# Optimization experiments

Measured on AMD Instinct MI355X. Metric: run time of the kernel, lower is better.

Reference implementation:

```python
import jax, jax.numpy as jnp
import numpy as np


def setup_inputs() -> dict:
    key = jax.random.key(0)
    x = jax.random.normal(key, (64, 512, 16, 16), dtype=jnp.float32)
    return {"x": x}


def reference(x):
    # x: [B, dim, h, w] -> covariance pooling y: [B, dim, dim]
    B, dim, h, w = x.shape
    M = h * w
    xf = x.reshape(B, dim, M)
    # I_hat = (1/M) I - (1/M^2) 11^T  (centering matrix scaled by 1/M)
    inv_M = jnp.asarray(1.0 / M, dtype=x.dtype)
    I_hat = inv_M * jnp.eye(M, dtype=x.dtype) - (inv_M * inv_M) * jnp.ones((M, M), dtype=x.dtype)
    # y = x @ I_hat @ x^T, I_hat broadcast over batch
    xI = jnp.einsum('bdm,mn->bdn', xf, I_hat)   # [B, dim, M]
    y = jnp.einsum('bdn,ben->bde', xI, xf)      # [B, dim, dim]
    return y
```

## Files before the change

### kernel.cpp

```cpp
#include <hip/hip_runtime.h>
#include <stdint.h>


typedef __attribute__((ext_vector_type(8))) short bf16x8;
typedef __attribute__((ext_vector_type(4))) float f32x4;

static __device__ __forceinline__ unsigned short f2bf(float f) {
    union { float f; uint32_t u; } c; c.f = f;
    uint32_t u = c.u;
    return (unsigned short)((u + 0x7FFFu + ((u >> 16) & 1u)) >> 16);
}

static __device__ __forceinline__ void cvt_store(f32x4 v0, f32x4 v1, float* psum,
                                                 unsigned short* dst) {
    v0 *= 0.0625f; v1 *= 0.0625f;
    *psum += (v0.x + v0.y + v0.z + v0.w) + (v1.x + v1.y + v1.z + v1.w);
    bf16x8 o;
    o[0] = (short)f2bf(v0.x); o[1] = (short)f2bf(v0.y);
    o[2] = (short)f2bf(v0.z); o[3] = (short)f2bf(v0.w);
    o[4] = (short)f2bf(v1.x); o[5] = (short)f2bf(v1.y);
    o[6] = (short)f2bf(v1.z); o[7] = (short)f2bf(v1.w);
    *(bf16x8*)dst = o;
}

__global__ __launch_bounds__(256) void covpool_fused(const float* __restrict__ x,
                                                     float* __restrict__ y) {
    __shared__ __align__(16) unsigned short As[128 * 32];
    __shared__ __align__(16) unsigned short Bs[128 * 32];
    __shared__ __align__(16) float Ep[32 * 132];
    __shared__ float muA[128];
    __shared__ float muB[128];

    const int xcd = blockIdx.x & 7;
    const int j   = blockIdx.x >> 3;
    const int b   = xcd * 8 + j / 10;
    const int t10 = j % 10;
    const unsigned code = (unsigned)((0xFBA7653210ULL >> (4 * t10)) & 15ULL);
    const int tm = code >> 2, tn = code & 3;
    const bool diag = (tm == tn);

    const float* Ag = x + ((size_t)b * 512 + tm * 128) * 256;
    const float* Bg = x + ((size_t)b * 512 + tn * 128) * 256;

    const int tid  = threadIdx.x;
    const int lane = tid & 63;
    const int wave = tid >> 6;
    const int wm = (wave >> 1) * 64;
    const int wn = (wave & 1) * 64;

    f32x4 acc[4][4] = {};
    float pA[2] = {0.f, 0.f}, pB[2] = {0.f, 0.f};

    const int rl  = lane & 15;
    const int q   = lane >> 4;
    const int swl = (q ^ ((rl >> 1) & 3)) * 8;
    const int srow = tid >> 2, schunk = tid & 3;

    f32x4 a0[2], a1[2], b0[2], b1[2];
#pragma unroll
    for (int t = 0; t < 2; ++t) {
        const float* g = Ag + (size_t)(t * 64 + srow) * 256 + schunk * 8;
        a0[t] = *(const f32x4*)g; a1[t] = *(const f32x4*)(g + 4);
        if (!diag) {
            const float* h = Bg + (size_t)(t * 64 + srow) * 256 + schunk * 8;
            b0[t] = *(const f32x4*)h; b1[t] = *(const f32x4*)(h + 4);
        }
    }

    for (int kk = 0; kk < 256; kk += 32) {
        __syncthreads();
#pragma unroll
        for (int t = 0; t < 2; ++t) {
            const int row  = t * 64 + srow;
            const int slot = schunk ^ ((row >> 1) & 3);
            cvt_store(a0[t], a1[t], &pA[t], As + row * 32 + slot * 8);
            if (!diag) cvt_store(b0[t], b1[t], &pB[t], Bs + row * 32 + slot * 8);
        }
        __syncthreads();
        if (kk < 224) {
#pragma unroll
            for (int t = 0; t < 2; ++t) {
                const float* g = Ag + (size_t)(t * 64 + srow) * 256 + (kk + 32) + schunk * 8;
                a0[t] = *(const f32x4*)g; a1[t] = *(const f32x4*)(g + 4);
                if (!diag) {
                    const float* h = Bg + (size_t)(t * 64 + srow) * 256 + (kk + 32) + schunk * 8;
                    b0[t] = *(const f32x4*)h; b1[t] = *(const f32x4*)(h + 4);
                }
            }
        }
        const unsigned short* Bsrc = diag ? As : Bs;
        bf16x8 af[4], bfr[4];
#pragma unroll
        for (int i = 0; i < 4; ++i)
            af[i] = *(const bf16x8*)(As + (wm + i * 16 + rl) * 32 + swl);
#pragma unroll
        for (int jj = 0; jj < 4; ++jj)
            bfr[jj] = *(const bf16x8*)(Bsrc + (wn + jj * 16 + rl) * 32 + swl);
#pragma unroll
        for (int i = 0; i < 4; ++i)
#pragma unroll
            for (int jj = 0; jj < 4; ++jj)
                acc[i][jj] = __builtin_amdgcn_mfma_f32_16x16x32_bf16(
                    af[i], bfr[jj], acc[i][jj], 0, 0, 0);
    }

#pragma unroll
    for (int t = 0; t < 2; ++t) {
        float s = pA[t];
        s += __shfl_xor(s, 1, 64); s += __shfl_xor(s, 2, 64);
        if (schunk == 0) muA[t * 64 + srow] = s * 0.0625f;
        if (!diag) {
            float sb = pB[t];
            sb += __shfl_xor(sb, 1, 64); sb += __shfl_xor(sb, 2, 64);
            if (schunk == 0) muB[t * 64 + srow] = sb * 0.0625f;
        }
    }
    const float* muBp = diag ? muA : muB;
    float* yb = y + (size_t)b * 512 * 512;

#pragma unroll
    for (int c = 0; c < 4; ++c) {
        __syncthreads();
        if ((wave >> 1) == (c >> 1)) {
            const int ii0 = 2 * (c & 1);
#pragma unroll
            for (int ii = 0; ii < 2; ++ii) {
                const int i = ii0 + ii;
#pragma unroll
                for (int jj = 0; jj < 4; ++jj) {
                    const int col = wn + jj * 16 + rl;
                    const float mb = muBp[col];
#pragma unroll
                    for (int r = 0; r < 4; ++r) {
                        const int row = wm + i * 16 + q * 4 + r;
                        Ep[(ii * 16 + q * 4 + r) * 132 + col] = acc[i][jj][r] - muA[row] * mb;
                    }
                }
            }
        }
        __syncthreads();
#pragma unroll
        for (int v = 0; v < 4; ++v) {
            const int flat = v * 256 + tid;
            const int rloc = flat >> 5, c4 = flat & 31;
            f32x4 val = *(const f32x4*)(Ep + rloc * 132 + c4 * 4);
            *(f32x4*)(yb + (size_t)(tm * 128 + c * 32 + rloc) * 512 + tn * 128 + c4 * 4) = val;
        }
        if (!diag) {
#pragma unroll
            for (int v = 0; v < 4; ++v) {
                const int id = v * 256 + tid;
                const int cc = id >> 3, g = id & 7;
                f32x4 val;
#pragma unroll
                for (int e = 0; e < 4; ++e)
                    val[e] = Ep[(g * 4 + e) * 132 + cc];
                *(f32x4*)(yb + (size_t)(tn * 128 + cc) * 512 + tm * 128 + c * 32 + g * 4) = val;
            }
        }
    }
}

extern "C" void kernel_launch(void* const* d_in, const int* in_sizes, int n_in,
                              void* d_out, int out_size, void* d_ws, size_t ws_size,
                              hipStream_t stream) {
    const float* x = (const float*)d_in[0];
    float* yout = (float*)d_out;
    (void)d_ws; (void)ws_size;
    covpool_fused<<<640, 256, 0, stream>>>(x, yout);
}
```

Measured before the change: 104.0 us.

## Use hardware packed bf16 convert, defer scaling to epilogue, raise occupancy bound

Replaces the software round-to-nearest bf16 conversion with the v_cvt_pk_bf16_f32 instruction, which packs two floats per instruction. The 1/16 pre-scaling of inputs before conversion is removed, and the 1/256 factor is applied once per output element in the epilogue instead. The launch bounds now request 3 waves per SIMD, and A fragments are loaded per row-tile inside the MFMA loop to reduce register pressure. Scaling after accumulation slightly changes rounding, and the tighter register budget may cause spills.

```diff
diff --git a/kernel.cpp b/kernel.cpp
--- a/kernel.cpp
+++ b/kernel.cpp
@@ -4,27 +4,27 @@
 
 typedef __attribute__((ext_vector_type(8))) short bf16x8;
 typedef __attribute__((ext_vector_type(4))) float f32x4;
+typedef __attribute__((ext_vector_type(4))) unsigned int u32x4;
 
-static __device__ __forceinline__ unsigned short f2bf(float f) {
-    union { float f; uint32_t u; } c; c.f = f;
-    uint32_t u = c.u;
-    return (unsigned short)((u + 0x7FFFu + ((u >> 16) & 1u)) >> 16);
+static __device__ __forceinline__ uint32_t cvtpk(float a, float b) {
+    uint32_t r;
+    asm("v_cvt_pk_bf16_f32 %0, %1, %2" : "=v"(r) : "v"(a), "v"(b));
+    return r;
 }
 
-static __device__ __forceinline__ void cvt_store(f32x4 v0, f32x4 v1, float* psum,
-                                                 unsigned short* dst) {
-    v0 *= 0.0625f; v1 *= 0.0625f;
+static __device__ __forceinline__ void stage8(f32x4 v0, f32x4 v1, float* psum,
+                                              unsigned short* dst) {
     *psum += (v0.x + v0.y + v0.z + v0.w) + (v1.x + v1.y + v1.z + v1.w);
-    bf16x8 o;
-    o[0] = (short)f2bf(v0.x); o[1] = (short)f2bf(v0.y);
-    o[2] = (short)f2bf(v0.z); o[3] = (short)f2bf(v0.w);
-    o[4] = (short)f2bf(v1.x); o[5] = (short)f2bf(v1.y);
-    o[6] = (short)f2bf(v1.z); o[7] = (short)f2bf(v1.w);
-    *(bf16x8*)dst = o;
+    u32x4 o;
+    o.x = cvtpk(v0.x, v0.y);
+    o.y = cvtpk(v0.z, v0.w);
+    o.z = cvtpk(v1.x, v1.y);
+    o.w = cvtpk(v1.z, v1.w);
+    *(u32x4*)dst = o;
 }
 
-__global__ __launch_bounds__(256) void covpool_fused(const float* __restrict__ x,
-                                                     float* __restrict__ y) {
+__global__ __launch_bounds__(256, 3) void covpool_fused(const float* __restrict__ x,
+                                                        float* __restrict__ y) {
     __shared__ __align__(16) unsigned short As[128 * 32];
     __shared__ __align__(16) unsigned short Bs[128 * 32];
     __shared__ __align__(16) float Ep[32 * 132];
@@ -73,8 +73,8 @@
         for (int t = 0; t < 2; ++t) {
             const int row  = t * 64 + srow;
             const int slot = schunk ^ ((row >> 1) & 3);
-            cvt_store(a0[t], a1[t], &pA[t], As + row * 32 + slot * 8);
-            if (!diag) cvt_store(b0[t], b1[t], &pB[t], Bs + row * 32 + slot * 8);
+            stage8(a0[t], a1[t], &pA[t], As + row * 32 + slot * 8);
+            if (!diag) stage8(b0[t], b1[t], &pB[t], Bs + row * 32 + slot * 8);
         }
         __syncthreads();
         if (kk < 224) {
@@ -89,34 +89,34 @@
             }
         }
         const unsigned short* Bsrc = diag ? As : Bs;
-        bf16x8 af[4], bfr[4];
-#pragma unroll
-        for (int i = 0; i < 4; ++i)
-            af[i] = *(const bf16x8*)(As + (wm + i * 16 + rl) * 32 + swl);
+        bf16x8 bfr[4];
 #pragma unroll
         for (int jj = 0; jj < 4; ++jj)
             bfr[jj] = *(const bf16x8*)(Bsrc + (wn + jj * 16 + rl) * 32 + swl);
 #pragma unroll
-        for (int i = 0; i < 4; ++i)
+        for (int i = 0; i < 4; ++i) {
+            const bf16x8 af = *(const bf16x8*)(As + (wm + i * 16 + rl) * 32 + swl);
 #pragma unroll
             for (int jj = 0; jj < 4; ++jj)
                 acc[i][jj] = __builtin_amdgcn_mfma_f32_16x16x32_bf16(
-                    af[i], bfr[jj], acc[i][jj], 0, 0, 0);
+                    af, bfr[jj], acc[i][jj], 0, 0, 0);
+        }
     }
 
 #pragma unroll
     for (int t = 0; t < 2; ++t) {
         float s = pA[t];
         s += __shfl_xor(s, 1, 64); s += __shfl_xor(s, 2, 64);
-        if (schunk == 0) muA[t * 64 + srow] = s * 0.0625f;
+        if (schunk == 0) muA[t * 64 + srow] = s * (1.0f / 256.0f);
         if (!diag) {
             float sb = pB[t];
             sb += __shfl_xor(sb, 1, 64); sb += __shfl_xor(sb, 2, 64);
-            if (schunk == 0) muB[t * 64 + srow] = sb * 0.0625f;
+            if (schunk == 0) muB[t * 64 + srow] = sb * (1.0f / 256.0f);
         }
     }
     const float* muBp = diag ? muA : muB;
     float* yb = y + (size_t)b * 512 * 512;
+    const float inv256 = 1.0f / 256.0f;
 
 #pragma unroll
     for (int c = 0; c < 4; ++c) {
@@ -133,7 +133,8 @@
 #pragma unroll
                     for (int r = 0; r < 4; ++r) {
                         const int row = wm + i * 16 + q * 4 + r;
-                        Ep[(ii * 16 + q * 4 + r) * 132 + col] = acc[i][jj][r] - muA[row] * mb;
+                        Ep[(ii * 16 + q * 4 + r) * 132 + col] =
+                            acc[i][jj][r] * inv256 - muA[row] * mb;
                     }
                 }
             }
```

After: 132.8 us. 27.7% more time.
